# Kernel optimization log

Measured on AMD Instinct MI355X. Metric: run time of the kernel, lower is better.

Reference implementation:

```python
import jax, jax.numpy as jnp
import numpy as np

B, N, FD, D, HF, WF = 4, 6, 256, 128, 64, 120
IMG_H, IMG_W = 480, 960
EPS_LN = 1e-5


def bilinear_sample(fmap, pts):
    """fmap: (B,C,H,W); pts: (B,P,2) xy pixel coords. Returns (B,P,C) values
    (zeros padding, align_corners=True convention) and (B,P) in-bounds mask."""
    Bc, C, H, W = fmap.shape
    flat = fmap.reshape(Bc, C, H * W)
    x, y = pts[..., 0], pts[..., 1]
    x0, y0 = jnp.floor(x), jnp.floor(y)
    out = jnp.zeros((Bc, pts.shape[1], C), fmap.dtype)
    for dx in (0.0, 1.0):
        for dy in (0.0, 1.0):
            cx, cy = x0 + dx, y0 + dy
            wgt = (1.0 - jnp.abs(x - cx)) * (1.0 - jnp.abs(y - cy))
            inb = (cx >= 0) & (cx <= W - 1) & (cy >= 0) & (cy <= H - 1)
            idx = (jnp.clip(cy, 0, H - 1) * W + jnp.clip(cx, 0, W - 1)).astype(jnp.int32)
            g = jnp.take_along_axis(flat, idx[:, None, :], axis=2)  # (B,C,P)
            out = out + (g * (wgt * inb)[:, None, :]).transpose(0, 2, 1)
    valid = (x >= 0) & (x <= W - 1) & (y >= 0) & (y <= H - 1)
    return out, valid


def _l2norm(x, axis):
    n = jnp.sqrt(jnp.sum(x * x, axis=axis, keepdims=True))
    return x / jnp.maximum(n, 1e-12)


def _ln(x, g, b):
    mu = jnp.mean(x, axis=-1, keepdims=True)
    var = jnp.mean((x - mu) ** 2, axis=-1, keepdims=True)
    return (x - mu) / jnp.sqrt(var + EPS_LN) * g + b


def setup_inputs() -> dict:
    key = jax.random.key(0)
    ks = jax.random.split(key, 12)
    rng = np.random.RandomState(0)
    feature = jax.random.normal(ks[0], (B, N, FD, HF, WF), jnp.float32)
    # realistic intrinsics (same K family for src/tar so homographies land in-frame)
    K = np.zeros((B, N, 3, 3), np.float32)
    K[..., 0, 0] = IMG_W * 0.8 * (1 + 0.01 * rng.randn(B, N))
    K[..., 1, 1] = IMG_W * 0.8 * (1 + 0.01 * rng.randn(B, N))
    K[..., 0, 2] = IMG_W / 2
    K[..., 1, 2] = IMG_H / 2
    K[..., 2, 2] = 1.0
    I_tar_inv = np.linalg.inv(K[:, 0]).astype(np.float32)  # (B,3,3)
    # extrinsics: near-identity rotation + small translation
    E = np.tile(np.eye(4, dtype=np.float32), (B, N, 1, 1))
    w = 0.02 * rng.randn(B, N, 3).astype(np.float32)
    skew = np.zeros((B, N, 3, 3), np.float32)
    skew[..., 0, 1], skew[..., 0, 2] = -w[..., 2], w[..., 1]
    skew[..., 1, 0], skew[..., 1, 2] = w[..., 2], -w[..., 0]
    skew[..., 2, 0], skew[..., 2, 1] = -w[..., 1], w[..., 0]
    E[..., :3, :3] = np.eye(3, dtype=np.float32) + skew
    E[..., :3, 3] = 0.1 * rng.randn(B, N, 3).astype(np.float32)
    nv = np.tile(np.array([0.0, -1.0, 0.0], np.float32), (B, 1, 1))
    nv += 0.01 * rng.randn(B, 1, 3).astype(np.float32)
    nv /= np.linalg.norm(nv, axis=-1, keepdims=True)
    sc_in, sc_hid = 1.0 / np.sqrt(FD), 1.0 / np.sqrt(D)
    return {
        "feature": feature,
        "I_src": jnp.asarray(K),
        "I_tar_inv": jnp.asarray(I_tar_inv),
        "E": jnp.asarray(E),
        "dis": jnp.float32(1.5),
        "norm_vec": jnp.asarray(nv),
        "bn_gamma": jnp.ones((FD,), jnp.float32),
        "bn_beta": jnp.zeros((FD,), jnp.float32),
        "bn_mean": jnp.zeros((FD,), jnp.float32),
        "bn_var": jnp.ones((FD,), jnp.float32),
        "conv_w": jax.random.normal(ks[1], (D, FD), jnp.float32) * sc_in,
        "ln1_g": jnp.ones((D,), jnp.float32),
        "ln1_b": jnp.zeros((D,), jnp.float32),
        "mlp_w1": jax.random.normal(ks[2], (D, 2 * D), jnp.float32) * sc_hid,
        "mlp_b1": jnp.zeros((2 * D,), jnp.float32),
        "mlp_w2": jax.random.normal(ks[3], (2 * D, D), jnp.float32) * sc_hid,
        "mlp_b2": jnp.zeros((D,), jnp.float32),
        "ln2_g": jnp.ones((D,), jnp.float32),
        "ln2_b": jnp.zeros((D,), jnp.float32),
    }


def reference(feature, I_src, I_tar_inv, E, dis, norm_vec, bn_gamma, bn_beta,
              bn_mean, bn_var, conv_w, ln1_g, ln1_b, mlp_w1, mlp_b1, mlp_w2,
              mlp_b2, ln2_g, ln2_b):
    b, n, fd, h, w = feature.shape
    d = conv_w.shape[0]
    P = h * w
    # feature_linear: BN (inference stats) + ReLU + 1x1 conv (no bias)
    f = (feature - bn_mean[:, None, None]) / jnp.sqrt(bn_var[:, None, None] + 1e-5)
    f = f * bn_gamma[:, None, None] + bn_beta[:, None, None]
    f = jax.nn.relu(f)
    val = jnp.einsum('of,bnfhw->bnohw', conv_w, f)  # (b,n,d,h,w)
    # homography of normalized grid scaled to image pixels
    xs = jnp.linspace(0.0, 1.0, w)
    ys = jnp.linspace(0.0, 1.0, h)
    X, Y = jnp.meshgrid(xs, ys)  # (h,w), xy indexing
    pix = jnp.stack([X.ravel() * IMG_W, Y.ravel() * IMG_H, jnp.ones(P)], 0)  # (3,P)
    R = E[..., :3, :3]
    T = E[..., :3, 3:]
    Hm = I_src @ (R - (T @ norm_vec[:, None]) / dis) @ I_tar_inv[:, None]  # (b,n,3,3)
    homo = jnp.einsum('bnij,jp->bnip', Hm, pix.astype(Hm.dtype))
    uv = homo[:, :, :2] / homo[:, :, 2:3]
    uv = uv / jnp.array([[IMG_W], [IMG_H]], uv.dtype)  # (b,n,2,P) in ~[0,1]
    # HomoGuideAttention
    pts = (uv * jnp.array([[w], [h]], uv.dtype)).transpose(0, 1, 3, 2).reshape(b * n, P, 2)
    sampled, valid = bilinear_sample(val.reshape(b * n, d, h, w), pts)  # (bn,P,d),(bn,P)
    keyv = _l2norm(sampled, axis=2).reshape(b, n, P, d)
    query = val[:, 0]  # (b,d,h,w)
    q = _l2norm(query.reshape(b, d, P), axis=1)
    dot = jnp.einsum('bdp,bnpd->bnp', q, keyv)
    dot = dot * valid.reshape(b, n, P).astype(dot.dtype)
    att = jax.nn.softmax(dot, axis=1)
    z = jnp.einsum('bnp,bnpd->bpd', att, sampled.reshape(b, n, P, d))
    z = z.transpose(0, 2, 1).reshape(b, d, h, w) + query
    z = z.reshape(b, d, P).transpose(0, 2, 1)  # (b,P,d)
    z = _ln(z, ln1_g, ln1_b)
    hmid = jax.nn.gelu(z @ mlp_w1 + mlp_b1, approximate=False)
    z = z + (hmid @ mlp_w2 + mlp_b2)
    z = _ln(z, ln2_g, ln2_b)
    return z.transpose(0, 2, 1).reshape(b, d, h, w)
```

## Files before the change

kernel.cpp:

```cpp
#include <hip/hip_runtime.h>
#include <hip/hip_bf16.h>
#include <math.h>

#define B_ 4
#define N_ 6
#define FD_ 256
#define D_ 128
#define HF_ 64
#define WF_ 120
#define P_ (HF_*WF_)

typedef __attribute__((ext_vector_type(8))) short short8;
typedef __attribute__((ext_vector_type(4))) float floatx4;
typedef __attribute__((ext_vector_type(4))) unsigned int uint4e;

__device__ inline float gred_sum(float v) {
  v += __shfl_xor(v, 1); v += __shfl_xor(v, 2);
  v += __shfl_xor(v, 4); v += __shfl_xor(v, 8);
  return v;
}

__device__ inline float gred32(float v) {
  v += __shfl_xor(v, 1); v += __shfl_xor(v, 2);
  v += __shfl_xor(v, 4); v += __shfl_xor(v, 8);
  v += __shfl_xor(v, 16);
  return v;
}

__device__ inline unsigned short f2bf(float f) {
  unsigned int u = __builtin_bit_cast(unsigned int, f);
  u += 0x7fffu + ((u >> 16) & 1u);
  return (unsigned short)(u >> 16);
}
__device__ inline float bf2f(unsigned short h) {
  return __builtin_bit_cast(float, ((unsigned int)h) << 16);
}
__device__ inline void bfu2(unsigned int u, float& lo, float& hi) {
  lo = __builtin_bit_cast(float, u << 16);
  hi = __builtin_bit_cast(float, u & 0xffff0000u);
}

__device__ inline unsigned int cvtpk_bf16(float lo, float hi) {
  unsigned int r;
  asm("v_cvt_pk_bf16_f32 %0, %1, %2" : "=v"(r) : "v"(lo), "v"(hi));
  return r;
}

__device__ inline void lds_barrier() {
  asm volatile("s_waitcnt lgkmcnt(0)\n\ts_barrier" ::: "memory");
}

__global__ __launch_bounds__(256) void setup_kernel(
    const float* __restrict__ I_src, const float* __restrict__ I_tar_inv,
    const float* __restrict__ E, const float* __restrict__ dis,
    const float* __restrict__ norm_vec,
    const float* __restrict__ conv_w, const float* __restrict__ w1,
    const float* __restrict__ w2,
    float2* __restrict__ uvbuf, unsigned short* __restrict__ wswz,
    unsigned short* __restrict__ w1s, unsigned short* __restrict__ w2s) {
  int bx = blockIdx.x;
  int tid = threadIdx.x;
  if (bx < 720) {
    int t = bx*256 + tid;
    int p  = t % P_;
    int bn = t / P_;
    int b  = bn / N_;
    const float* e  = E + bn*16;
    const float* nv = norm_vec + b*3;
    float inv_dis = 1.0f / dis[0];
    float M[9];
    #pragma unroll
    for (int r = 0; r < 3; r++)
      #pragma unroll
      for (int c = 0; c < 3; c++)
        M[r*3+c] = e[r*4+c] - e[r*4+3]*nv[c]*inv_dis;
    const float* Is = I_src + bn*9;
    float A[9];
    #pragma unroll
    for (int r = 0; r < 3; r++)
      #pragma unroll
      for (int c = 0; c < 3; c++)
        A[r*3+c] = Is[r*3+0]*M[0*3+c] + Is[r*3+1]*M[1*3+c] + Is[r*3+2]*M[2*3+c];
    const float* It = I_tar_inv + b*9;
    float H[9];
    #pragma unroll
    for (int r = 0; r < 3; r++)
      #pragma unroll
      for (int c = 0; c < 3; c++)
        H[r*3+c] = A[r*3+0]*It[0*3+c] + A[r*3+1]*It[1*3+c] + A[r*3+2]*It[2*3+c];
    int py = p / WF_, px = p - py*WF_;
    float pixx = (float)px * (960.f/119.f);
    float pixy = (float)py * (480.f/63.f);
    float hx = H[0]*pixx + H[1]*pixy + H[2];
    float hy = H[3]*pixx + H[4]*pixy + H[5];
    float hz = H[6]*pixx + H[7]*pixy + H[8];
    float sx = (hx/hz) * ((float)WF_/960.f);
    float sy = (hy/hz) * ((float)HF_/480.f);
    uvbuf[t] = make_float2(sx, sy);
  } else if (bx < 848) {
    int t = (bx-720)*256 + tid;
    int j    =  t        & 7;
    int lane = (t >> 3)  & 63;
    int dt   = (t >> 9)  & 7;
    int kc   =  t >> 12;
    int d = dt*16 + (lane & 15);
    int k = kc*32 + (lane >> 4)*8 + j;
    wswz[t] = f2bf(conv_w[d*FD_ + k]);
  } else {
    int t = (bx-848)*256 + tid;
    if (t < 32768) {
      int j    =  t        & 7;
      int lane = (t >> 3)  & 63;
      int dt   = (t >> 9)  & 15;
      int kc   =  t >> 13;
      int n = dt*16 + (lane & 15);
      int k = kc*32 + (lane >> 4)*8 + j;
      w1s[t] = f2bf(w1[k*256 + n]);
    } else {
      int u = t - 32768;
      int j    =  u        & 7;
      int lane = (u >> 3)  & 63;
      int dt   = (u >> 9)  & 7;
      int kc   =  u >> 12;
      int n = dt*16 + (lane & 15);
      int k = kc*32 + (lane >> 4)*8 + j;
      w2s[u] = f2bf(w2[k*128 + n]);
    }
  }
}

#define AST_ 36
__global__ __launch_bounds__(256) void conv_kernel(const float* __restrict__ feature,
    const unsigned short* __restrict__ wswz,
    const float* __restrict__ bn_gamma, const float* __restrict__ bn_beta,
    const float* __restrict__ bn_mean, const float* __restrict__ bn_var,
    unsigned short* __restrict__ val) {
  __shared__ __align__(16) char csm[19968];
  unsigned short* apadA = (unsigned short*)csm;
  unsigned short* apadB = (unsigned short*)(csm + 4608);
  unsigned short* ytile = (unsigned short*)csm;
  float* sbn = (float*)(csm + 17408);

  int tid = threadIdx.x;
  {
    float s = bn_gamma[tid] * rsqrtf(bn_var[tid] + 1e-5f);
    sbn[tid] = s;
    sbn[256+tid] = bn_beta[tid] - bn_mean[tid] * s;
  }

  int bn = blockIdx.y;
  int p0 = blockIdx.x * 64;
  const float* fbase2 = feature + (size_t)bn*FD_*P_ + p0;

  int K0 = tid >> 4;
  int sp = (tid & 15) * 4;

  int ln = tid & 63, wv = tid >> 6;
  int m = ln & 15, q = ln >> 4;
  int row = wv*16 + m;

  float4 va[2], vb[2];
  {
    const float* fb0 = fbase2 + (size_t)(2*K0)*P_ + sp;
    va[0] = *(const float4*)fb0; vb[0] = *(const float4*)(fb0 + P_);
    const float* fb1 = fbase2 + (size_t)(32 + 2*K0)*P_ + sp;
    va[1] = *(const float4*)fb1; vb[1] = *(const float4*)(fb1 + P_);
  }
  __syncthreads();

  floatx4 acc[8];
  #pragma unroll
  for (int dt = 0; dt < 8; dt++) acc[dt] = (floatx4){0.f,0.f,0.f,0.f};

  {
    int k0 = 0;
    float s0 = sbn[k0+2*K0],   b0 = sbn[256+k0+2*K0];
    float s1 = sbn[k0+2*K0+1], b1 = sbn[256+k0+2*K0+1];
    float a0[4] = {va[0].x, va[0].y, va[0].z, va[0].w};
    float a1[4] = {vb[0].x, vb[0].y, vb[0].z, vb[0].w};
    #pragma unroll
    for (int i = 0; i < 4; i++) {
      unsigned int w = cvtpk_bf16(fmaxf(a0[i]*s0+b0, 0.f),
                                  fmaxf(a1[i]*s1+b1, 0.f));
      *(unsigned int*)&apadA[(sp+i)*AST_ + 2*K0] = w;
    }
  }

  #pragma unroll
  for (int kc = 0; kc < 8; kc++) {
    lds_barrier();
    if (kc + 2 < 8) {
      const float* fb = fbase2 + (size_t)((kc+2)*32 + 2*K0)*P_ + sp;
      va[kc&1] = *(const float4*)fb;
      vb[kc&1] = *(const float4*)(fb + P_);
    }
    if (kc + 1 < 8) {
      int s = (kc+1)&1;
      int k0 = (kc+1)*32;
      unsigned short* ap = ((kc+1)&1) ? apadB : apadA;
      float s0 = sbn[k0+2*K0],   b0 = sbn[256+k0+2*K0];
      float s1 = sbn[k0+2*K0+1], b1 = sbn[256+k0+2*K0+1];
      float a0[4] = {va[s].x, va[s].y, va[s].z, va[s].w};
      float a1[4] = {vb[s].x, vb[s].y, vb[s].z, vb[s].w};
      #pragma unroll
      for (int i = 0; i < 4; i++) {
        unsigned int w = cvtpk_bf16(fmaxf(a0[i]*s0+b0, 0.f),
                                    fmaxf(a1[i]*s1+b1, 0.f));
        *(unsigned int*)&ap[(sp+i)*AST_ + 2*K0] = w;
      }
    }
    unsigned short* rp = (kc&1) ? apadB : apadA;
    uint2 u0 = *(const uint2*)&rp[row*AST_ + q*8];
    uint2 u1 = *(const uint2*)&rp[row*AST_ + q*8 + 4];
    uint4e ua = {u0.x, u0.y, u1.x, u1.y};
    short8 af = __builtin_bit_cast(short8, ua);
    #pragma unroll
    for (int dt = 0; dt < 8; dt++) {
      short8 bfg = *(const short8*)(wswz + (((size_t)kc*8 + dt)*64 + ln)*8);
      acc[dt] = __builtin_amdgcn_mfma_f32_16x16x32_bf16(af, bfg, acc[dt], 0, 0, 0);
    }
  }
  __syncthreads();

  #pragma unroll
  for (int dt = 0; dt < 8; dt++)
    #pragma unroll
    for (int r = 0; r < 4; r++)
      ytile[(wv*16 + q*4 + r)*136 + dt*16 + m] = f2bf(acc[dt][r]);
  __syncthreads();
  #pragma unroll
  for (int i = 0; i < 4; i++) {
    int idx = tid + i*256;
    int pp = idx >> 4, ch = idx & 15;
    uint4 v = *(const uint4*)&ytile[pp*136 + ch*8];
    *(uint4*)(val + ((size_t)bn*P_ + p0 + pp)*D_ + ch*8) = v;
  }
}

__global__ __launch_bounds__(256, 4) void attmlp_kernel(
    const unsigned short* __restrict__ val, const float2* __restrict__ uvbuf,
    const float* __restrict__ ln1_g, const float* __restrict__ ln1_b,
    const unsigned short* __restrict__ w1s, const float* __restrict__ b1,
    const unsigned short* __restrict__ w2s, const float* __restrict__ b2,
    const float* __restrict__ ln2_g, const float* __restrict__ ln2_b,
    float* __restrict__ out) {
  __shared__ __align__(16) char smem[26112];
  unsigned short* zt = (unsigned short*)smem;
  unsigned short* ht = (unsigned short*)(smem + 8704);
  float* lnp = (float*)(smem + 25600);
  float* yt = (float*)smem;

  int tid = threadIdx.x;
  int b = blockIdx.y;
  int bx = blockIdx.x;
  int tile = (bx & 7) * 30 + (bx >> 3);
  int p0 = tile * 32;
  int ln = tid & 63, wv = tid >> 6;

  {
    int grp = ln >> 5, c = ln & 31;
    float g1[4], be1[4];
    *(float4*)&g1[0]  = *(const float4*)(ln1_g + c*4);
    *(float4*)&be1[0] = *(const float4*)(ln1_b + c*4);

    for (int pass = 0; pass < 4; pass++) {
      int pl = pass*8 + wv*2 + grp;
      int p = p0 + pl;

      uint2 qu = *(const uint2*)(val + ((size_t)(b*N_)*P_ + p)*D_ + c*4);
      float qv[4];
      bfu2(qu.x, qv[0], qv[1]); bfu2(qu.y, qv[2], qv[3]);
      float qp = 0.f;
      #pragma unroll
      for (int i = 0; i < 4; i++) qp += qv[i]*qv[i];
      float qinv = 1.f / fmaxf(sqrtf(gred32(qp)), 1e-12f);

      float dotv[N_];
      float sv[N_][4];
      #pragma unroll
      for (int np = 0; np < 3; np++) {
        uint2 g[2][4]; float wm[2][4]; bool vld[2];
        #pragma unroll
        for (int t = 0; t < 2; t++) {
          int n = np*2 + t;
          float2 uv = uvbuf[((size_t)(b*N_ + n))*P_ + p];
          float sx = uv.x, sy = uv.y;
          float x0f = floorf(sx), y0f = floorf(sy);
          float fx = sx - x0f, fy = sy - y0f;
          int x0 = (int)x0f, y0 = (int)y0f;
          const unsigned short* base = val + ((size_t)(b*N_+n)*P_)*D_ + c*4;
          #pragma unroll
          for (int k = 0; k < 4; k++) {
            int dx = k & 1, dy = k >> 1;
            int cx = x0 + dx, cy = y0 + dy;
            bool inb = (cx >= 0) && (cx <= WF_-1) && (cy >= 0) && (cy <= HF_-1);
            int icx = min(max(cx,0),WF_-1), icy = min(max(cy,0),HF_-1);
            wm[t][k] = inb ? (dx ? fx : 1.f-fx) * (dy ? fy : 1.f-fy) : 0.f;
            g[t][k] = *(const uint2*)(base + (size_t)(icy*WF_ + icx)*D_);
          }
          vld[t] = (sx >= 0.f) && (sx <= (float)(WF_-1)) && (sy >= 0.f) && (sy <= (float)(HF_-1));
        }
        #pragma unroll
        for (int t = 0; t < 2; t++) {
          int n = np*2 + t;
          float acc[4];
          #pragma unroll
          for (int i = 0; i < 4; i++) acc[i] = 0.f;
          #pragma unroll
          for (int k = 0; k < 4; k++) {
            float gg[4];
            bfu2(g[t][k].x, gg[0], gg[1]); bfu2(g[t][k].y, gg[2], gg[3]);
            float w = wm[t][k];
            #pragma unroll
            for (int i = 0; i < 4; i++) acc[i] += gg[i]*w;
          }
          float ssp = 0.f, qsp = 0.f;
          #pragma unroll
          for (int i = 0; i < 4; i++) { ssp += acc[i]*acc[i]; qsp += qv[i]*acc[i]; }
          float ss = gred32(ssp);
          float qs = gred32(qsp);
          float dn = qs * qinv / fmaxf(sqrtf(ss), 1e-12f);
          dotv[n] = vld[t] ? dn : 0.f;
          #pragma unroll
          for (int i = 0; i < 4; i++) sv[n][i] = acc[i];
        }
      }
      float mx = dotv[0];
      #pragma unroll
      for (int n = 1; n < N_; n++) mx = fmaxf(mx, dotv[n]);
      float e[N_]; float den = 0.f;
      #pragma unroll
      for (int n = 0; n < N_; n++) { e[n] = expf(dotv[n]-mx); den += e[n]; }
      float rden = 1.f/den;
      float z[4];
      #pragma unroll
      for (int i = 0; i < 4; i++) z[i] = qv[i];
      #pragma unroll
      for (int n = 0; n < N_; n++) {
        float a = e[n]*rden;
        #pragma unroll
        for (int i = 0; i < 4; i++) z[i] += a*sv[n][i];
      }
      float sp = 0.f;
      #pragma unroll
      for (int i = 0; i < 4; i++) sp += z[i];
      float mu = gred32(sp) * (1.f/128.f);
      float vp = 0.f;
      #pragma unroll
      for (int i = 0; i < 4; i++) { float d0 = z[i]-mu; vp += d0*d0; }
      float rs = rsqrtf(gred32(vp) * (1.f/128.f) + 1e-5f);
      unsigned int ow[2];
      #pragma unroll
      for (int i = 0; i < 2; i++) {
        float o0 = (z[2*i]-mu)*rs*g1[2*i] + be1[2*i];
        float o1 = (z[2*i+1]-mu)*rs*g1[2*i+1] + be1[2*i+1];
        ow[i] = (unsigned int)f2bf(o0) | ((unsigned int)f2bf(o1) << 16);
      }
      *(uint2*)&zt[pl*136 + c*4] = make_uint2(ow[0], ow[1]);
    }
  }
  __syncthreads();

  int m = ln & 15, q = ln >> 4;
  int h = wv >> 1, ch2 = wv & 1;

  floatx4 a1[8];
  #pragma unroll
  for (int j = 0; j < 8; j++) a1[j] = (floatx4){0.f,0.f,0.f,0.f};
  #pragma unroll
  for (int kc = 0; kc < 4; kc++) {
    short8 af = *(const short8*)&zt[(h*16+m)*136 + kc*32 + q*8];
    #pragma unroll
    for (int j = 0; j < 8; j++) {
      int dt = ch2*8 + j;
      short8 bfg = *(const short8*)(w1s + (((size_t)kc*16 + dt)*64 + ln)*8);
      a1[j] = __builtin_amdgcn_mfma_f32_16x16x32_bf16(af, bfg, a1[j], 0, 0, 0);
    }
  }
  #pragma unroll
  for (int j = 0; j < 8; j++) {
    int dt = ch2*8 + j;
    float bb = b1[dt*16 + m];
    #pragma unroll
    for (int r = 0; r < 4; r++) {
      float x = a1[j][r] + bb;
      float hv = 0.5f*x*(1.f + erff(x*0.70710678118654752f));
      ht[(h*16 + q*4 + r)*264 + dt*16 + m] = f2bf(hv);
    }
  }
  __syncthreads();

  floatx4 a2[4];
  #pragma unroll
  for (int j = 0; j < 4; j++) a2[j] = (floatx4){0.f,0.f,0.f,0.f};
  #pragma unroll
  for (int kc = 0; kc < 8; kc++) {
    short8 af = *(const short8*)&ht[(h*16+m)*264 + kc*32 + q*8];
    #pragma unroll
    for (int j = 0; j < 4; j++) {
      int dt = ch2*4 + j;
      short8 bfg = *(const short8*)(w2s + (((size_t)kc*8 + dt)*64 + ln)*8);
      a2[j] = __builtin_amdgcn_mfma_f32_16x16x32_bf16(af, bfg, a2[j], 0, 0, 0);
    }
  }
  float y[4][4];
  #pragma unroll
  for (int j = 0; j < 4; j++) {
    int dt = ch2*4 + j;
    float bb = b2[dt*16 + m];
    #pragma unroll
    for (int r = 0; r < 4; r++) {
      int pp = h*16 + q*4 + r;
      y[j][r] = a2[j][r] + bb + bf2f(zt[pp*136 + dt*16 + m]);
    }
  }
  #pragma unroll
  for (int r = 0; r < 4; r++) {
    float sp = 0.f, sq = 0.f;
    #pragma unroll
    for (int j = 0; j < 4; j++) { sp += y[j][r]; sq += y[j][r]*y[j][r]; }
    sp = gred_sum(sp); sq = gred_sum(sq);
    if (m == 0) {
      int pl = h*16 + q*4 + r;
      lnp[(ch2*32 + pl)*2 + 0] = sp;
      lnp[(ch2*32 + pl)*2 + 1] = sq;
    }
  }
  __syncthreads();
  float mu_[4], rs_[4];
  #pragma unroll
  for (int r = 0; r < 4; r++) {
    int pl = h*16 + q*4 + r;
    float sum = lnp[pl*2]     + lnp[(32+pl)*2];
    float ssq = lnp[pl*2 + 1] + lnp[(32+pl)*2 + 1];
    float mu = sum * (1.f/128.f);
    float var = fmaxf(ssq * (1.f/128.f) - mu*mu, 0.f);
    mu_[r] = mu; rs_[r] = rsqrtf(var + 1e-5f);
  }
  float gg[4], be[4];
  #pragma unroll
  for (int j = 0; j < 4; j++) {
    int d = (ch2*4 + j)*16 + m;
    gg[j] = ln2_g[d]; be[j] = ln2_b[d];
  }
  #pragma unroll
  for (int j = 0; j < 4; j++)
    #pragma unroll
    for (int r = 0; r < 4; r++)
      y[j][r] = (y[j][r] - mu_[r])*rs_[r]*gg[j] + be[j];
  __syncthreads();
  #pragma unroll
  for (int j = 0; j < 4; j++)
    #pragma unroll
    for (int r = 0; r < 4; r++)
      yt[((ch2*4 + j)*16 + m)*34 + h*16 + q*4 + r] = y[j][r];
  __syncthreads();

  #pragma unroll
  for (int i = 0; i < 8; i++) {
    int idx = tid + i*256;
    int d = idx >> 4, pu = idx & 15;
    *(float2*)(out + ((size_t)(b*D_ + d))*P_ + p0 + pu*2) = *(float2*)&yt[d*34 + pu*2];
  }
}

extern "C" void kernel_launch(void* const* d_in, const int* in_sizes, int n_in,
                              void* d_out, int out_size, void* d_ws, size_t ws_size,
                              hipStream_t stream) {
  (void)in_sizes; (void)n_in; (void)out_size; (void)ws_size;
  const float* feature   = (const float*)d_in[0];
  const float* I_src     = (const float*)d_in[1];
  const float* I_tar_inv = (const float*)d_in[2];
  const float* E         = (const float*)d_in[3];
  const float* dis       = (const float*)d_in[4];
  const float* norm_vec  = (const float*)d_in[5];
  const float* bn_gamma  = (const float*)d_in[6];
  const float* bn_beta   = (const float*)d_in[7];
  const float* bn_mean   = (const float*)d_in[8];
  const float* bn_var    = (const float*)d_in[9];
  const float* conv_w    = (const float*)d_in[10];
  const float* ln1_g     = (const float*)d_in[11];
  const float* ln1_b     = (const float*)d_in[12];
  const float* mlp_w1    = (const float*)d_in[13];
  const float* mlp_b1    = (const float*)d_in[14];
  const float* mlp_w2    = (const float*)d_in[15];
  const float* mlp_b2    = (const float*)d_in[16];
  const float* ln2_g     = (const float*)d_in[17];
  const float* ln2_b     = (const float*)d_in[18];
  float* out = (float*)d_out;

  char* ws = (char*)d_ws;
  unsigned short* wswz = (unsigned short*)(ws + 0);
  unsigned short* w1s  = (unsigned short*)(ws + 65536);
  unsigned short* w2s  = (unsigned short*)(ws + 131072);
  float2* uvbuf        = (float2*)(ws + 196608);
  unsigned short* val  = (unsigned short*)(ws + 1671168);

  hipLaunchKernelGGL(setup_kernel, dim3(1104), dim3(256), 0, stream,
                     I_src, I_tar_inv, E, dis, norm_vec,
                     conv_w, mlp_w1, mlp_w2,
                     uvbuf, wswz, w1s, w2s);
  hipLaunchKernelGGL(conv_kernel, dim3(120, 24), dim3(256), 0, stream,
                     feature, wswz, bn_gamma, bn_beta, bn_mean, bn_var, val);
  hipLaunchKernelGGL(attmlp_kernel, dim3(240, 4), dim3(256), 0, stream,
                     val, uvbuf, ln1_g, ln1_b,
                     w1s, mlp_b1, w2s, mlp_b2, ln2_g, ln2_b, out);
}
```

Baseline: 354.7 us.

## Load conv A-fragments straight from global, dropping LDS staging and barriers

```diff
diff --git a/kernel.cpp b/kernel.cpp
--- a/kernel.cpp
+++ b/kernel.cpp
@@ -44,10 +44,6 @@
   unsigned int r;
   asm("v_cvt_pk_bf16_f32 %0, %1, %2" : "=v"(r) : "v"(lo), "v"(hi));
   return r;
-}
-
-__device__ inline void lds_barrier() {
-  asm volatile("s_waitcnt lgkmcnt(0)\n\ts_barrier" ::: "memory");
 }
 
 __global__ __launch_bounds__(256) void setup_kernel(
@@ -129,90 +125,56 @@
   }
 }
 
-#define AST_ 36
 __global__ __launch_bounds__(256) void conv_kernel(const float* __restrict__ feature,
     const unsigned short* __restrict__ wswz,
     const float* __restrict__ bn_gamma, const float* __restrict__ bn_beta,
     const float* __restrict__ bn_mean, const float* __restrict__ bn_var,
     unsigned short* __restrict__ val) {
-  __shared__ __align__(16) char csm[19968];
-  unsigned short* apadA = (unsigned short*)csm;
-  unsigned short* apadB = (unsigned short*)(csm + 4608);
+  __shared__ __align__(16) char csm[19456];
   unsigned short* ytile = (unsigned short*)csm;
   float* sbn = (float*)(csm + 17408);
 
   int tid = threadIdx.x;
   {
-    float s = bn_gamma[tid] * rsqrtf(bn_var[tid] + 1e-5f);
-    sbn[tid] = s;
-    sbn[256+tid] = bn_beta[tid] - bn_mean[tid] * s;
+    float sc = bn_gamma[tid] * rsqrtf(bn_var[tid] + 1e-5f);
+    sbn[tid] = sc;
+    sbn[256+tid] = bn_beta[tid] - bn_mean[tid] * sc;
   }
 
   int bn = blockIdx.y;
   int p0 = blockIdx.x * 64;
-  const float* fbase2 = feature + (size_t)bn*FD_*P_ + p0;
-
-  int K0 = tid >> 4;
-  int sp = (tid & 15) * 4;
 
   int ln = tid & 63, wv = tid >> 6;
   int m = ln & 15, q = ln >> 4;
   int row = wv*16 + m;
 
-  float4 va[2], vb[2];
-  {
-    const float* fb0 = fbase2 + (size_t)(2*K0)*P_ + sp;
-    va[0] = *(const float4*)fb0; vb[0] = *(const float4*)(fb0 + P_);
-    const float* fb1 = fbase2 + (size_t)(32 + 2*K0)*P_ + sp;
-    va[1] = *(const float4*)fb1; vb[1] = *(const float4*)(fb1 + P_);
-  }
+  const float* fb = feature + (size_t)bn*FD_*P_ + p0 + row;
+
   __syncthreads();
 
   floatx4 acc[8];
   #pragma unroll
   for (int dt = 0; dt < 8; dt++) acc[dt] = (floatx4){0.f,0.f,0.f,0.f};
 
-  {
-    int k0 = 0;
-    float s0 = sbn[k0+2*K0],   b0 = sbn[256+k0+2*K0];
-    float s1 = sbn[k0+2*K0+1], b1 = sbn[256+k0+2*K0+1];
-    float a0[4] = {va[0].x, va[0].y, va[0].z, va[0].w};
-    float a1[4] = {vb[0].x, vb[0].y, vb[0].z, vb[0].w};
-    #pragma unroll
-    for (int i = 0; i < 4; i++) {
-      unsigned int w = cvtpk_bf16(fmaxf(a0[i]*s0+b0, 0.f),
-                                  fmaxf(a1[i]*s1+b1, 0.f));
-      *(unsigned int*)&apadA[(sp+i)*AST_ + 2*K0] = w;
-    }
-  }
-
   #pragma unroll
   for (int kc = 0; kc < 8; kc++) {
-    lds_barrier();
-    if (kc + 2 < 8) {
-      const float* fb = fbase2 + (size_t)((kc+2)*32 + 2*K0)*P_ + sp;
-      va[kc&1] = *(const float4*)fb;
-      vb[kc&1] = *(const float4*)(fb + P_);
-    }
-    if (kc + 1 < 8) {
-      int s = (kc+1)&1;
-      int k0 = (kc+1)*32;
-      unsigned short* ap = ((kc+1)&1) ? apadB : apadA;
-      float s0 = sbn[k0+2*K0],   b0 = sbn[256+k0+2*K0];
-      float s1 = sbn[k0+2*K0+1], b1 = sbn[256+k0+2*K0+1];
-      float a0[4] = {va[s].x, va[s].y, va[s].z, va[s].w};
-      float a1[4] = {vb[s].x, vb[s].y, vb[s].z, vb[s].w};
-      #pragma unroll
-      for (int i = 0; i < 4; i++) {
-        unsigned int w = cvtpk_bf16(fmaxf(a0[i]*s0+b0, 0.f),
-                                    fmaxf(a1[i]*s1+b1, 0.f));
-        *(unsigned int*)&ap[(sp+i)*AST_ + 2*K0] = w;
-      }
-    }
-    unsigned short* rp = (kc&1) ? apadB : apadA;
-    uint2 u0 = *(const uint2*)&rp[row*AST_ + q*8];
-    uint2 u1 = *(const uint2*)&rp[row*AST_ + q*8 + 4];
-    uint4e ua = {u0.x, u0.y, u1.x, u1.y};
+    int kbase = kc*32 + q*8;
+    float fv[8];
+    #pragma unroll
+    for (int j = 0; j < 8; j++)
+      fv[j] = fb[(size_t)(kbase + j)*P_];
+    float4 sA = *(const float4*)&sbn[kbase];
+    float4 sB = *(const float4*)&sbn[kbase+4];
+    float4 bA = *(const float4*)&sbn[256+kbase];
+    float4 bB = *(const float4*)&sbn[256+kbase+4];
+    float ss[8] = {sA.x,sA.y,sA.z,sA.w,sB.x,sB.y,sB.z,sB.w};
+    float bb[8] = {bA.x,bA.y,bA.z,bA.w,bB.x,bB.y,bB.z,bB.w};
+    unsigned int wpk[4];
+    #pragma unroll
+    for (int i = 0; i < 4; i++)
+      wpk[i] = cvtpk_bf16(fmaxf(fv[2*i]*ss[2*i]+bb[2*i], 0.f),
+                          fmaxf(fv[2*i+1]*ss[2*i+1]+bb[2*i+1], 0.f));
+    uint4e ua = {wpk[0], wpk[1], wpk[2], wpk[3]};
     short8 af = __builtin_bit_cast(short8, ua);
     #pragma unroll
     for (int dt = 0; dt < 8; dt++) {
@@ -220,7 +182,6 @@
       acc[dt] = __builtin_amdgcn_mfma_f32_16x16x32_bf16(af, bfg, acc[dt], 0, 0, 0);
     }
   }
-  __syncthreads();
 
   #pragma unroll
   for (int dt = 0; dt < 8; dt++)
```

After: 368.4 us. +3.9%, slower.
